# Kernel optimization log

Measured on AMD Instinct MI355X. Metric: run time of the kernel, lower is better.

Reference implementation:

```python
import jax, jax.numpy as jnp
import numpy as np

FILTER_SIZE = 27           # filter_size (K + 2)
K = FILTER_SIZE - 2        # sampled neighbors per central node
FEAT = 512                 # feature_dim
HID = 512                  # hidden_dim
NUM_NODES = 100000         # node-id universe for the features() embedding
B = 20000                  # batch of central nodes
ALPHA = 0.2                # leaky relu slope


def _star_eigvec(fs):
    # eigenvectors of I - D A D for the star graph on `fs` nodes (node 0 = hub)
    A = np.zeros((fs, fs))
    A[0, 1:] = 1.0
    A[1:, 0] = 1.0
    D = np.eye(fs)
    D[0, 0] = (fs - 1) ** (-0.5)
    L = np.eye(fs) - D @ A @ D
    _, u = np.linalg.eigh(L)
    return u.astype(np.float32)


def setup_inputs() -> dict:
    key = jax.random.key(0)
    k1, k2, k3, k4, k5 = jax.random.split(key, 5)
    nodes = jax.random.randint(k1, (B,), 0, NUM_NODES)
    neigh = jax.random.randint(k2, (B, K), 0, NUM_NODES)
    feat_table = jax.random.normal(k3, (NUM_NODES, FEAT), dtype=jnp.float32)
    # xavier_uniform for W [FEAT, HID] and a [2*HID]
    limW = float(np.sqrt(6.0 / (FEAT + HID)))
    W = jax.random.uniform(k4, (FEAT, HID), minval=-limW, maxval=limW, dtype=jnp.float32)
    lima = float(np.sqrt(6.0 / (1 + 2 * HID)))
    a_vec = jax.random.uniform(k5, (2 * HID,), minval=-lima, maxval=lima, dtype=jnp.float32)
    U = jnp.asarray(_star_eigvec(FILTER_SIZE))
    return {"nodes": nodes, "neigh": neigh, "feat_table": feat_table,
            "W": W, "a_vec": a_vec, "U": U}


def reference(nodes, neigh, feat_table, W, a_vec, U):
    # project features: input2 (central), input1 (neighbors)
    h_ct = feat_table[nodes] @ W                              # [B, H]
    h_nb = jnp.einsum('bkf,fh->bkh', feat_table[neigh], W)    # [B, K, H]
    # GAT-style edge scores: a @ [h_ct ; h_nb]
    s_ct = h_ct @ a_vec[:HID]                                 # [B]
    s_nb = h_nb @ a_vec[HID:]                                 # [B, K]
    logits = s_ct[:, None] + s_nb                             # [B, K]
    lrelu = jnp.where(logits > 0, logits, ALPHA * logits)
    edge_e = jnp.exp(-lrelu)                                  # [B, K]
    # per-row normalization (equals dense a1 rowsum: neighbors per row distinct)
    attn = edge_e / jnp.sum(edge_e, axis=1, keepdims=True)    # [B, K]
    # mask1: slots 1..K of each filter_size block hold attn * h_nb
    mask = attn[..., None] * h_nb                             # [B, K, H]
    m = jnp.pad(mask, ((0, 0), (1, 1), (0, 0)))               # [B, FILTER_SIZE, H]
    mt = jnp.swapaxes(m, 1, 2)                                # [B, H, FILTER_SIZE]
    # spectral transform: (mt @ U @ U^T) @ ones[FILTER_SIZE,1]
    avg = jnp.ones((FILTER_SIZE, 1), dtype=m.dtype)
    temp = ((mt @ U) @ U.T) @ avg                             # [B, H, 1]
    out = jnp.squeeze(temp, axis=-1)                          # [B, H]
    return jax.nn.relu(out)
```

## Files before the change

### kernel.cpp

```cpp
#include <hip/hip_runtime.h>
#include <stdint.h>
#include <string.h>

#define FEAT 512
#define HID 512
#define KNB 25
#define FS 27
#define NNODES 100000
#define ALPHA 0.2f

typedef short bf16x8 __attribute__((ext_vector_type(8)));
typedef float f32x4 __attribute__((ext_vector_type(4)));

__device__ __forceinline__ float bf2f(unsigned short u) {
    union { unsigned int i; float f; } x; x.i = ((unsigned int)u) << 16; return x.f;
}
__device__ __forceinline__ unsigned short f2bf(float f) {
    unsigned int x = __float_as_uint(f);
    unsigned int r = (x + 0x7fffu + ((x >> 16) & 1u)) >> 16;
    return (unsigned short)r;
}
__device__ __forceinline__ float ldf(const void* base, size_t idx, bool isf32) {
    return isf32 ? ((const float*)base)[idx] : bf2f(((const unsigned short*)base)[idx]);
}

__global__ void detect_dtype(const void* __restrict__ feat, int* __restrict__ flag) {
    __shared__ int cnt;
    if (threadIdx.x == 0) cnt = 0;
    __syncthreads();
    const unsigned short* u = (const unsigned short*)feat;
    int c = 0;
    for (int i = threadIdx.x; i < 2048; i += 256) {
        float av = fabsf(bf2f(u[i]));
        if (!(av < 1e4f)) c++;
    }
    atomicAdd(&cnt, c);
    __syncthreads();
    if (threadIdx.x == 0) *flag = (cnt > 16) ? 1 : 0;
}

__global__ void prep_pq(const void* __restrict__ W, const void* __restrict__ a_vec,
                        const int* __restrict__ flag,
                        float* __restrict__ p, float* __restrict__ q) {
    bool isf32 = (*flag != 0);
    int f = blockIdx.x;
    int lane = threadIdx.x;
    float accp = 0.f, accq = 0.f;
    #pragma unroll
    for (int j = 0; j < 8; ++j) {
        int h = lane * 8 + j;
        float wv = ldf(W, (size_t)f * HID + h, isf32);
        accq += wv * ldf(a_vec, h, isf32);
        accp += wv * ldf(a_vec, HID + h, isf32);
    }
    #pragma unroll
    for (int off = 32; off > 0; off >>= 1) {
        accp += __shfl_down(accp, off);
        accq += __shfl_down(accq, off);
    }
    if (lane == 0) { p[f] = accp; q[f] = accq; }
}

__global__ void prep_M(const void* __restrict__ U, const int* __restrict__ flag,
                       float* __restrict__ Mv) {
    __shared__ float cs[FS];
    bool isf32 = (*flag != 0);
    int t = threadIdx.x;
    if (t < FS) {
        float c = 0.f;
        for (int i = 0; i < FS; ++i) c += ldf(U, i * FS + t, isf32);
        cs[t] = c;
    }
    __syncthreads();
    if (t < FS) {
        float m = 0.f;
        for (int j = 0; j < FS; ++j) m += ldf(U, t * FS + j, isf32) * cs[j];
        Mv[t] = m;
    }
}

__global__ void transposeW(const void* __restrict__ W, const int* __restrict__ flag,
                           unsigned short* __restrict__ Wt) {
    bool isf32 = (*flag != 0);
    int idx = blockIdx.x * blockDim.x + threadIdx.x;
    int n = idx >> 9, k = idx & (HID - 1);
    Wt[idx] = f2bf(ldf(W, (size_t)k * HID + n, isf32));
}

__global__ __launch_bounds__(256) void convert_score(
    const void* __restrict__ feat, const float* __restrict__ p,
    const float* __restrict__ q, const int* __restrict__ flag,
    unsigned short* __restrict__ featbf, float* __restrict__ sp,
    float* __restrict__ sq, int nRows) {
    bool isf32 = (*flag != 0);
    int wave = threadIdx.x >> 6, lane = threadIdx.x & 63;
    int row = blockIdx.x * 4 + wave;
    if (row >= nRows) return;
    float vals[8];
    if (isf32) {
        const float4* src = (const float4*)((const float*)feat + (size_t)row * FEAT) + lane * 2;
        float4 v0 = src[0], v1 = src[1];
        vals[0] = v0.x; vals[1] = v0.y; vals[2] = v0.z; vals[3] = v0.w;
        vals[4] = v1.x; vals[5] = v1.y; vals[6] = v1.z; vals[7] = v1.w;
        unsigned short o[8];
        #pragma unroll
        for (int j = 0; j < 8; ++j) o[j] = f2bf(vals[j]);
        *(uint4*)(&featbf[(size_t)row * FEAT + lane * 8]) = *(const uint4*)o;
    } else {
        uint4 v = *((const uint4*)((const unsigned short*)feat + (size_t)row * FEAT) + lane);
        unsigned int w4[4] = {v.x, v.y, v.z, v.w};
        #pragma unroll
        for (int j = 0; j < 4; ++j) {
            vals[2 * j]     = __uint_as_float(w4[j] << 16);
            vals[2 * j + 1] = __uint_as_float(w4[j] & 0xffff0000u);
        }
    }
    float accp = 0.f, accq = 0.f;
    const float* pv = p + lane * 8;
    const float* qv = q + lane * 8;
    #pragma unroll
    for (int j = 0; j < 8; ++j) { accp += vals[j] * pv[j]; accq += vals[j] * qv[j]; }
    #pragma unroll
    for (int off = 32; off > 0; off >>= 1) {
        accp += __shfl_down(accp, off);
        accq += __shfl_down(accq, off);
    }
    if (lane == 0) { sp[row] = accp; sq[row] = accq; }
}

__global__ __launch_bounds__(256) void attn_gather2(
    const void* __restrict__ feat, const unsigned short* __restrict__ featbf,
    const int* __restrict__ nodes, const int* __restrict__ neigh,
    const float* __restrict__ sp, const float* __restrict__ sq,
    const float* __restrict__ Mv, const int* __restrict__ flag,
    unsigned short* __restrict__ g, int B) {
    bool isf32 = (*flag != 0);
    const unsigned short* F = isf32 ? featbf : (const unsigned short*)feat;
    int wave = threadIdx.x >> 6, lane = threadIdx.x & 63;
    int b = blockIdx.x * 4 + wave;
    if (b >= B) return;
    int id = 0; float e = 0.f;
    if (lane < KNB) {
        id = neigh[(size_t)b * KNB + lane];
        float l = sq[nodes[b]] + sp[id];
        float lr = l > 0.f ? l : ALPHA * l;
        e = __expf(-lr);
    }
    float Z = e;
    #pragma unroll
    for (int off = 16; off > 0; off >>= 1) Z += __shfl_down(Z, off);
    Z = __shfl(Z, 0);
    float w = (lane < KNB) ? e * (1.f / Z) * Mv[lane + 1] : 0.f;
    float acc[8] = {0.f, 0.f, 0.f, 0.f, 0.f, 0.f, 0.f, 0.f};
    #pragma unroll
    for (int k = 0; k < KNB; ++k) {
        int idk = __builtin_amdgcn_readlane(id, k);
        float wk = __uint_as_float((unsigned int)__builtin_amdgcn_readlane(__float_as_int(w), k));
        uint4 v = *((const uint4*)(F + (size_t)idk * FEAT) + lane);
        unsigned int w4[4] = {v.x, v.y, v.z, v.w};
        #pragma unroll
        for (int j = 0; j < 4; ++j) {
            acc[2 * j]     += wk * __uint_as_float(w4[j] << 16);
            acc[2 * j + 1] += wk * __uint_as_float(w4[j] & 0xffff0000u);
        }
    }
    unsigned short o[8];
    #pragma unroll
    for (int j = 0; j < 8; ++j) o[j] = f2bf(acc[j]);
    *(uint4*)(&g[(size_t)b * FEAT + lane * 8]) = *(const uint4*)o;
}

__global__ __launch_bounds__(256) void attn_gather(
    const void* __restrict__ feat, const int* __restrict__ nodes,
    const int* __restrict__ neigh, const float* __restrict__ p,
    const float* __restrict__ q, const float* __restrict__ Mv,
    const int* __restrict__ flag, unsigned short* __restrict__ g) {
    __shared__ __attribute__((aligned(16))) unsigned short ldsF[KNB * FEAT];
    __shared__ float ldsS[KNB + 1];
    bool isf32 = (*flag != 0);
    int b = blockIdx.x;
    int t = threadIdx.x;
    int wave = t >> 6, lane = t & 63;
    for (int r = wave; r < KNB + 1; r += 4) {
        int id = (r == 0) ? nodes[b] : neigh[(size_t)b * KNB + (r - 1)];
        float vals[8];
        if (isf32) {
            const float4* row = (const float4*)((const float*)feat + (size_t)id * FEAT) + lane * 2;
            float4 v0 = row[0], v1 = row[1];
            vals[0] = v0.x; vals[1] = v0.y; vals[2] = v0.z; vals[3] = v0.w;
            vals[4] = v1.x; vals[5] = v1.y; vals[6] = v1.z; vals[7] = v1.w;
        } else {
            uint4 v = *((const uint4*)((const unsigned short*)feat + (size_t)id * FEAT) + lane);
            unsigned int w4[4] = {v.x, v.y, v.z, v.w};
            #pragma unroll
            for (int j = 0; j < 4; ++j) {
                vals[2 * j]     = bf2f((unsigned short)(w4[j] & 0xffffu));
                vals[2 * j + 1] = bf2f((unsigned short)(w4[j] >> 16));
            }
        }
        if (r > 0) {
            unsigned short o[8];
            #pragma unroll
            for (int j = 0; j < 8; ++j) o[j] = f2bf(vals[j]);
            *(uint4*)(&ldsF[(r - 1) * FEAT + lane * 8]) = *(const uint4*)o;
        }
        const float* vec = ((r == 0) ? q : p) + lane * 8;
        float acc = 0.f;
        #pragma unroll
        for (int j = 0; j < 8; ++j) acc += vals[j] * vec[j];
        #pragma unroll
        for (int off = 32; off > 0; off >>= 1) acc += __shfl_down(acc, off);
        if (lane == 0) ldsS[r] = acc;
    }
    __syncthreads();
    float s0 = ldsS[0];
    float w[KNB];
    float Z = 0.f;
    #pragma unroll
    for (int k = 0; k < KNB; ++k) {
        float l = s0 + ldsS[k + 1];
        float lr = l > 0.f ? l : ALPHA * l;
        float e = __expf(-lr);
        w[k] = e;
        Z += e;
    }
    float inv = 1.f / Z;
    #pragma unroll
    for (int k = 0; k < KNB; ++k) w[k] *= inv * Mv[k + 1];
    float acc0 = 0.f, acc1 = 0.f;
    #pragma unroll
    for (int k = 0; k < KNB; ++k) {
        unsigned int v = *(const unsigned int*)(&ldsF[k * FEAT + 2 * t]);
        acc0 += w[k] * bf2f((unsigned short)(v & 0xffffu));
        acc1 += w[k] * bf2f((unsigned short)(v >> 16));
    }
    unsigned int o = ((unsigned int)f2bf(acc1) << 16) | (unsigned int)f2bf(acc0);
    *(unsigned int*)(&g[(size_t)b * FEAT + 2 * t]) = o;
}

__global__ __launch_bounds__(256) void gemm_relu(
    const unsigned short* __restrict__ G, const unsigned short* __restrict__ Wt,
    const int* __restrict__ flag, void* __restrict__ out, int M) {
    __shared__ __attribute__((aligned(16))) unsigned short As[64 * 72];
    __shared__ __attribute__((aligned(16))) unsigned short Bs[64 * 72];
    bool isf32 = (*flag != 0);
    int t = threadIdx.x;
    int mBase = blockIdx.y * 64;
    int nBase = blockIdx.x * 64;
    int wave = t >> 6, lane = t & 63;
    int mOff = (wave & 1) * 32, nOff = (wave >> 1) * 32;
    f32x4 acc00 = {0.f, 0.f, 0.f, 0.f}, acc01 = {0.f, 0.f, 0.f, 0.f};
    f32x4 acc10 = {0.f, 0.f, 0.f, 0.f}, acc11 = {0.f, 0.f, 0.f, 0.f};
    int lr = t >> 2;
    int seg = (t & 3) * 16;
    int fr = lane & 15, quad = lane >> 4;
    for (int k0 = 0; k0 < FEAT; k0 += 64) {
        uint4 av0 = {0u, 0u, 0u, 0u}, av1 = {0u, 0u, 0u, 0u};
        int gr = mBase + lr;
        if (gr < M) {
            const unsigned short* s = G + (size_t)gr * FEAT + k0 + seg;
            av0 = *(const uint4*)s;
            av1 = *(const uint4*)(s + 8);
        }
        *(uint4*)(&As[lr * 72 + seg]) = av0;
        *(uint4*)(&As[lr * 72 + seg + 8]) = av1;
        const unsigned short* bs = Wt + (size_t)(nBase + lr) * FEAT + k0 + seg;
        *(uint4*)(&Bs[lr * 72 + seg]) = *(const uint4*)bs;
        *(uint4*)(&Bs[lr * 72 + seg + 8]) = *(const uint4*)(bs + 8);
        __syncthreads();
        #pragma unroll
        for (int kk = 0; kk < 64; kk += 32) {
            bf16x8 a0 = *(const bf16x8*)(&As[(mOff + fr) * 72 + kk + quad * 8]);
            bf16x8 a1 = *(const bf16x8*)(&As[(mOff + 16 + fr) * 72 + kk + quad * 8]);
            bf16x8 b0 = *(const bf16x8*)(&Bs[(nOff + fr) * 72 + kk + quad * 8]);
            bf16x8 b1 = *(const bf16x8*)(&Bs[(nOff + 16 + fr) * 72 + kk + quad * 8]);
            acc00 = __builtin_amdgcn_mfma_f32_16x16x32_bf16(a0, b0, acc00, 0, 0, 0);
            acc01 = __builtin_amdgcn_mfma_f32_16x16x32_bf16(a0, b1, acc01, 0, 0, 0);
            acc10 = __builtin_amdgcn_mfma_f32_16x16x32_bf16(a1, b0, acc10, 0, 0, 0);
            acc11 = __builtin_amdgcn_mfma_f32_16x16x32_bf16(a1, b1, acc11, 0, 0, 0);
        }
        __syncthreads();
    }
    int col = lane & 15, qr = (lane >> 4) * 4;
    #pragma unroll
    for (int sel = 0; sel < 4; ++sel) {
        f32x4 a = (sel == 0) ? acc00 : (sel == 1) ? acc01 : (sel == 2) ? acc10 : acc11;
        int mt = sel >> 1, nt = sel & 1;
        #pragma unroll
        for (int i = 0; i < 4; ++i) {
            int row = mBase + mOff + mt * 16 + qr + i;
            if (row < M) {
                int cn = nBase + nOff + nt * 16 + col;
                float v = a[i];
                v = v > 0.f ? v : 0.f;
                size_t off = (size_t)row * HID + cn;
                if (isf32) ((float*)out)[off] = v;
                else ((unsigned short*)out)[off] = f2bf(v);
            }
        }
    }
}

extern "C" void kernel_launch(void* const* d_in, const int* in_sizes, int n_in,
                              void* d_out, int out_size, void* d_ws, size_t ws_size,
                              hipStream_t stream) {
    const int* nodes = (const int*)d_in[0];
    const int* neigh = (const int*)d_in[1];
    const void* feat = d_in[2];
    const void* W = d_in[3];
    const void* a_vec = d_in[4];
    const void* U = d_in[5];
    int B = in_sizes[0];

    char* ws = (char*)d_ws;
    int* flag = (int*)ws;
    float* p = (float*)(ws + 256);
    float* q = (float*)(ws + 256 + 2048);
    float* Mv = (float*)(ws + 256 + 4096);
    unsigned short* Wt = (unsigned short*)(ws + 4608);
    unsigned short* g = (unsigned short*)(ws + 4608 + (size_t)FEAT * HID * 2);
    size_t gEnd = 4608 + (size_t)FEAT * HID * 2 + (size_t)B * FEAT * 2;
    float* sp = (float*)(ws + gEnd);
    float* sq = (float*)(ws + gEnd + (size_t)NNODES * 4);
    unsigned short* featbf = (unsigned short*)(ws + gEnd + (size_t)NNODES * 8);
    size_t need = gEnd + (size_t)NNODES * 8 + (size_t)NNODES * FEAT * 2;

    detect_dtype<<<1, 256, 0, stream>>>(feat, flag);
    prep_pq<<<FEAT, 64, 0, stream>>>(W, a_vec, flag, p, q);
    prep_M<<<1, 32, 0, stream>>>(U, flag, Mv);
    transposeW<<<(FEAT * HID) / 256, 256, 0, stream>>>(W, flag, Wt);
    if (ws_size >= need) {
        convert_score<<<(NNODES + 3) / 4, 256, 0, stream>>>(feat, p, q, flag, featbf, sp, sq, NNODES);
        attn_gather2<<<(B + 3) / 4, 256, 0, stream>>>(feat, featbf, nodes, neigh, sp, sq, Mv, flag, g, B);
    } else {
        attn_gather<<<B, 256, 0, stream>>>(feat, nodes, neigh, p, q, Mv, flag, g);
    }
    dim3 gg(HID / 64, (B + 63) / 64);
    gemm_relu<<<gg, 256, 0, stream>>>(g, Wt, flag, d_out, B);
}
```

Measured before the change: 426.1 us.

## Add 128x128-tile MFMA GEMM with direct global-to-LDS loads

Adds a new bf16 GEMM+ReLU kernel for the fast path. It uses 128x128 output tiles, each wave computing a 64x64 sub-tile with 4x4 MFMA 16x16x32 accumulators. Operands are staged through global_load_lds 16-byte direct-to-LDS transfers, which skip register round-trips. The larger tiles are meant to raise operand reuse and cut global traffic compared with the 64x64 kernel. The trade-offs are unpadded LDS rows that may cause bank conflicts on fragment reads, higher register pressure, and out-of-range row reads on the last M tile; only the stores are guarded.

```diff
diff --git a/kernel.cpp b/kernel.cpp
--- a/kernel.cpp
+++ b/kernel.cpp
@@ -22,6 +22,11 @@
 }
 __device__ __forceinline__ float ldf(const void* base, size_t idx, bool isf32) {
     return isf32 ? ((const float*)base)[idx] : bf2f(((const unsigned short*)base)[idx]);
+}
+__device__ __forceinline__ void gload16(const void* g, void* lds) {
+    __builtin_amdgcn_global_load_lds(
+        (const __attribute__((address_space(1))) unsigned int*)g,
+        (__attribute__((address_space(3))) unsigned int*)lds, 16, 0, 0);
 }
 
 __global__ void detect_dtype(const void* __restrict__ feat, int* __restrict__ flag) {
@@ -236,6 +241,72 @@
     }
     unsigned int o = ((unsigned int)f2bf(acc1) << 16) | (unsigned int)f2bf(acc0);
     *(unsigned int*)(&g[(size_t)b * FEAT + 2 * t]) = o;
+}
+
+__global__ __launch_bounds__(256) void gemm_relu128(
+    const unsigned short* __restrict__ G, const unsigned short* __restrict__ Wt,
+    const int* __restrict__ flag, void* __restrict__ out, int M) {
+    __shared__ __attribute__((aligned(16))) unsigned short As[128 * 64];
+    __shared__ __attribute__((aligned(16))) unsigned short Bs[128 * 64];
+    bool isf32 = (*flag != 0);
+    int t = threadIdx.x;
+    int wave = t >> 6, lane = t & 63;
+    int mBase = blockIdx.y * 128;
+    int nBase = blockIdx.x * 128;
+    int wr = wave >> 1, wc = wave & 1;
+    int fr = lane & 15, quad = lane >> 4;
+    f32x4 acc[4][4];
+    #pragma unroll
+    for (int m = 0; m < 4; ++m)
+        #pragma unroll
+        for (int n = 0; n < 4; ++n) acc[m][n] = (f32x4){0.f, 0.f, 0.f, 0.f};
+
+    int lrow = lane >> 3;
+    int lcol = (lane & 7) * 8;
+    for (int k0 = 0; k0 < FEAT; k0 += 64) {
+        #pragma unroll
+        for (int i = 0; i < 4; ++i) {
+            int r = wave * 32 + i * 8;
+            gload16(G + (size_t)(mBase + r + lrow) * FEAT + k0 + lcol, &As[r * 64]);
+            gload16(Wt + (size_t)(nBase + r + lrow) * FEAT + k0 + lcol, &Bs[r * 64]);
+        }
+        __syncthreads();
+        #pragma unroll
+        for (int kk = 0; kk < 64; kk += 32) {
+            bf16x8 av[4], bv[4];
+            #pragma unroll
+            for (int m = 0; m < 4; ++m)
+                av[m] = *(const bf16x8*)(&As[(wr * 64 + m * 16 + fr) * 64 + kk + quad * 8]);
+            #pragma unroll
+            for (int n = 0; n < 4; ++n)
+                bv[n] = *(const bf16x8*)(&Bs[(wc * 64 + n * 16 + fr) * 64 + kk + quad * 8]);
+            #pragma unroll
+            for (int m = 0; m < 4; ++m)
+                #pragma unroll
+                for (int n = 0; n < 4; ++n)
+                    acc[m][n] = __builtin_amdgcn_mfma_f32_16x16x32_bf16(av[m], bv[n], acc[m][n], 0, 0, 0);
+        }
+        __syncthreads();
+    }
+    int col = lane & 15, qr = (lane >> 4) * 4;
+    #pragma unroll
+    for (int m = 0; m < 4; ++m) {
+        #pragma unroll
+        for (int n = 0; n < 4; ++n) {
+            #pragma unroll
+            for (int i = 0; i < 4; ++i) {
+                int row = mBase + wr * 64 + m * 16 + qr + i;
+                if (row < M) {
+                    int cn = nBase + wc * 64 + n * 16 + col;
+                    float v = acc[m][n][i];
+                    v = v > 0.f ? v : 0.f;
+                    size_t off = (size_t)row * HID + cn;
+                    if (isf32) ((float*)out)[off] = v;
+                    else ((unsigned short*)out)[off] = f2bf(v);
+                }
+            }
+        }
+    }
 }
 
 __global__ __launch_bounds__(256) void gemm_relu(
@@ -332,9 +403,11 @@
     if (ws_size >= need) {
         convert_score<<<(NNODES + 3) / 4, 256, 0, stream>>>(feat, p, q, flag, featbf, sp, sq, NNODES);
         attn_gather2<<<(B + 3) / 4, 256, 0, stream>>>(feat, featbf, nodes, neigh, sp, sq, Mv, flag, g, B);
+        dim3 gg(HID / 128, (B + 127) / 128);
+        gemm_relu128<<<gg, 256, 0, stream>>>(g, Wt, flag, d_out, B);
     } else {
         attn_gather<<<B, 256, 0, stream>>>(feat, nodes, neigh, p, q, Mv, flag, g);
-    }
-    dim3 gg(HID / 64, (B + 63) / 64);
-    gemm_relu<<<gg, 256, 0, stream>>>(g, Wt, flag, d_out, B);
-}
+        dim3 gg(HID / 64, (B + 63) / 64);
+        gemm_relu<<<gg, 256, 0, stream>>>(g, Wt, flag, d_out, B);
+    }
+}
```

After: 428.2 us. No clear change (+0.5%).
